# Kernel tuning notes

Hardware: AMD Instinct MI355X
Metric: run time of the kernel (lower is better)

The kernel has to match this reference:

```python
import jax, jax.numpy as jnp
import numpy as np

N = 50000   # nodes
E = 500000  # edges
DIN = 128
DOUT = 128
H = 8       # mulhead
DH = DOUT // H
L = 2       # layers per branch
NC = 7      # emotion classes
EPS = 1e-9  # BatchNorm eps from source


def _bn(x):
    # BatchNorm1d in train mode, gamma=1/beta=0 at init
    m = x.mean(axis=0)
    v = x.var(axis=0)
    return (x - m) * jax.lax.rsqrt(v + EPS)


def _gat_forward(f, row, col, vals, Ws, bs, Wn, bn, As, An):
    for i in range(L):
        hs = jax.nn.relu(jnp.einsum('nd,hdk->nhk', f, Ws[i]) + bs[i])  # [N,H,DH]
        hn = jax.nn.relu(jnp.einsum('nd,hdk->nhk', f, Wn[i]) + bn[i])  # [N,H,DH]
        ats = jax.nn.leaky_relu(jnp.einsum('nhk,hk->nh', hs, As[i]), negative_slope=0.2)  # [N,H]
        # NOTE: source computes attention_neigh from f_self (faithful)
        atn = jax.nn.leaky_relu(jnp.einsum('nhk,hk->nh', hs, An[i]), negative_slope=0.2)  # [N,H]
        e = (ats[row] + atn[col]) * vals[:, None]            # [E,H] per-edge attention
        msg = e[:, :, None] * hn[col]                        # [E,H,DH] gather + weight
        agg = jax.ops.segment_sum(msg, row, num_segments=N)  # [N,H,DH] scatter-add (sparse mm)
        f = _bn(agg.reshape(N, H * DH))                      # concat heads + norm
    return f


def _gcn_forward(f, row, col, vals, W, b):
    for i in range(L):
        h = f @ W[i] + b[i]                                  # [N,DOUT]
        agg = jax.ops.segment_sum(vals[:, None] * h[col], row, num_segments=N)
        f = _bn(jax.nn.relu(agg))
    return f


def setup_inputs() -> dict:
    key = jax.random.key(0)
    ks = jax.random.split(key, 24)
    inp = {}
    inp['f_in'] = jax.random.normal(ks[0], (N, DIN), jnp.float32)
    inp['edge_row'] = jax.random.randint(ks[1], (E,), 0, N, jnp.int32)
    inp['edge_col'] = jax.random.randint(ks[2], (E,), 0, N, jnp.int32)
    inp['vals_gat'] = jax.random.uniform(ks[3], (E,), jnp.float32)
    inp['vals_uttr'] = jax.random.uniform(ks[4], (E,), jnp.float32)
    inp['vals_past'] = jax.random.uniform(ks[5], (E,), jnp.float32)
    inp['vals_futr'] = jax.random.uniform(ks[6], (E,), jnp.float32)
    s = 0.05
    # GAT params (stacked over [layer, head]); layer0 in=DIN, later in=DOUT (equal here)
    inp['gat_Ws'] = jax.random.normal(ks[7], (L, H, DIN, DH), jnp.float32) * s
    inp['gat_bs'] = jnp.zeros((L, H, DH), jnp.float32)
    inp['gat_Wn'] = jax.random.normal(ks[8], (L, H, DIN, DH), jnp.float32) * s
    inp['gat_bn'] = jnp.zeros((L, H, DH), jnp.float32)
    inp['gat_as'] = jnp.ones((L, H, DH), jnp.float32)  # init ones per source
    inp['gat_an'] = jnp.ones((L, H, DH), jnp.float32)
    # three vanilla GCN branches
    inp['W_uttr'] = jax.random.normal(ks[9], (L, DIN, DOUT), jnp.float32) * s
    inp['b_uttr'] = jnp.zeros((L, DOUT), jnp.float32)
    inp['W_past'] = jax.random.normal(ks[10], (L, DIN, DOUT), jnp.float32) * s
    inp['b_past'] = jnp.zeros((L, DOUT), jnp.float32)
    inp['W_futr'] = jax.random.normal(ks[11], (L, DIN, DOUT), jnp.float32) * s
    inp['b_futr'] = jnp.zeros((L, DOUT), jnp.float32)
    # self perceptron + classifier
    inp['W_self'] = jax.random.normal(ks[12], (DIN, DOUT), jnp.float32) * s
    inp['b_self'] = jnp.zeros((DOUT,), jnp.float32)
    inp['W_cls'] = jax.random.normal(ks[13], (5 * DOUT, NC), jnp.float32) * s
    inp['b_cls'] = jnp.zeros((NC,), jnp.float32)
    return inp


def reference(f_in, edge_row, edge_col, vals_gat, vals_uttr, vals_past, vals_futr,
              gat_Ws, gat_bs, gat_Wn, gat_bn, gat_as, gat_an,
              W_uttr, b_uttr, W_past, b_past, W_futr, b_futr,
              W_self, b_self, W_cls, b_cls):
    o_gat = _gat_forward(f_in, edge_row, edge_col, vals_gat,
                         gat_Ws, gat_bs, gat_Wn, gat_bn, gat_as, gat_an)
    o_uttr = _gcn_forward(f_in, edge_row, edge_col, vals_uttr, W_uttr, b_uttr)
    o_past = _gcn_forward(f_in, edge_row, edge_col, vals_past, W_past, b_past)
    o_futr = _gcn_forward(f_in, edge_row, edge_col, vals_futr, W_futr, b_futr)
    o_self = _bn(jax.nn.relu(f_in @ W_self + b_self))
    f = jnp.concatenate([o_gat, o_uttr, o_past, o_futr, o_self], axis=1)  # [N,640]
    return f @ W_cls + b_cls  # classifier: act=False, plain linear
```

## Files before the change

kernel.cpp:

```cpp
#include <hip/hip_runtime.h>
#include <hip/hip_bf16.h>


#define NN 50000
#define NE 500000
#define DD 128
#define NH 8
#define DHD 16
#define NCLS 7
#define SCAN_B 196

typedef __attribute__((ext_vector_type(8))) short short8;
typedef __attribute__((ext_vector_type(4))) float f32x4;

__device__ __forceinline__ unsigned short f2bf(float x) {
    unsigned int u = __float_as_uint(x);
    unsigned int r = (u + 0x7fffu + ((u >> 16) & 1u)) >> 16;
    return (unsigned short)r;
}
__device__ __forceinline__ unsigned int pack2bf(float lo, float hi) {
    return (unsigned int)f2bf(lo) | ((unsigned int)f2bf(hi) << 16);
}
__device__ __forceinline__ float bflo(unsigned int u) { return __uint_as_float(u << 16); }
__device__ __forceinline__ float bfhi(unsigned int u) { return __uint_as_float(u & 0xffff0000u); }


__global__ void count_kernel(const int* __restrict__ row, int* __restrict__ cnt) {
    int e = blockIdx.x * 256 + threadIdx.x;
    if (e < NE) atomicAdd(&cnt[row[e]], 1);
}

__global__ __launch_bounds__(256) void scan1_kernel(const int* __restrict__ cnt,
                                                    int* __restrict__ pre,
                                                    int* __restrict__ bsum) {
    __shared__ int s[256];
    int t = threadIdx.x;
    int i = blockIdx.x * 256 + t;
    int v = (i < NN) ? cnt[i] : 0;
    s[t] = v;
    __syncthreads();
    for (int off = 1; off < 256; off <<= 1) {
        int u = (t >= off) ? s[t - off] : 0;
        __syncthreads();
        s[t] += u;
        __syncthreads();
    }
    if (i < NN) pre[i] = s[t] - v;
    if (t == 255) bsum[blockIdx.x] = s[255];
}

__global__ __launch_bounds__(256) void scan2_kernel(const int* __restrict__ bsum,
                                                    int* __restrict__ boff) {
    __shared__ int s[256];
    int t = threadIdx.x;
    int v = (t < SCAN_B) ? bsum[t] : 0;
    s[t] = v;
    __syncthreads();
    for (int off = 1; off < 256; off <<= 1) {
        int u = (t >= off) ? s[t - off] : 0;
        __syncthreads();
        s[t] += u;
        __syncthreads();
    }
    boff[t] = s[t] - v;
    if (t == 255) boff[256] = s[255];
}

__global__ __launch_bounds__(256) void scan3_kernel(const int* __restrict__ pre,
                                                    const int* __restrict__ boff,
                                                    int* __restrict__ row_ptr,
                                                    int* __restrict__ fill) {
    int t = threadIdx.x;
    int i = blockIdx.x * 256 + t;
    if (i < NN) {
        int v = pre[i] + boff[blockIdx.x];
        row_ptr[i] = v;
        fill[i] = v;
    }
    if (blockIdx.x == 0 && t == 0) row_ptr[NN] = boff[256];
}

__global__ void scatter_kernel(const int* __restrict__ row, const int* __restrict__ col,
                               const float* __restrict__ vg, const float* __restrict__ vu,
                               const float* __restrict__ vp, const float* __restrict__ vf,
                               int* __restrict__ fill, int4* __restrict__ ed) {
    int e = blockIdx.x * 256 + threadIdx.x;
    if (e >= NE) return;
    int r = row[e];
    int pos = atomicAdd(&fill[r], 1);
    ed[2 * pos] = make_int4(col[e], __float_as_int(vg[e]), __float_as_int(vu[e]),
                            __float_as_int(vp[e]));
    ed[2 * pos + 1] = make_int4(__float_as_int(vf[e]), 0, 0, 0);
}


__global__ __launch_bounds__(256) void tobf16_kernel(const float* __restrict__ x,
                                                     short* __restrict__ y) {
    int idx = blockIdx.x * 256 + threadIdx.x;
    if (idx >= NN * DD / 8) return;
    float4 a = ((const float4*)x)[idx * 2];
    float4 b = ((const float4*)x)[idx * 2 + 1];
    uint4 o;
    o.x = pack2bf(a.x, a.y);
    o.y = pack2bf(a.z, a.w);
    o.z = pack2bf(b.x, b.y);
    o.w = pack2bf(b.z, b.w);
    *(uint4*)(y + (size_t)idx * 8) = o;
}


struct WPrepArgs {
    const float* src[11];
};

__global__ __launch_bounds__(256) void wprep_kernel(WPrepArgs a, short* __restrict__ out) {
    int idx = blockIdx.x * 256 + threadIdx.x;
    if (idx >= 11 * DD * DD) return;
    int w = idx >> 14;
    int r = idx & 16383;
    int n = r >> 7, k = r & 127;
    const float* W = a.src[w];
    float v = (w < 4) ? W[(size_t)((n >> 4) * DD + k) * DHD + (n & 15)] : W[(size_t)k * DD + n];
    out[idx] = (short)f2bf(v);
}


struct WFixArgs {
    const float* W1[3];
    const float* b1[3];
    const float* stats[3];
};

__global__ __launch_bounds__(256) void wfix_kernel(WFixArgs a, short* __restrict__ wt_out,
                                                   float* __restrict__ bfix) {
    int idx = blockIdx.x * 256 + threadIdx.x;
    if (idx >= 3 * DD) return;
    int br = idx >> 7, n = idx & 127;
    const float* st = a.stats[br];
    const float* W = a.W1[br];
    const float inv_n = 1.0f / (float)NN;
    float accb = 0.f;
    short* wo = wt_out + (size_t)br * DD * DD + (size_t)n * DD;
#pragma unroll 4
    for (int k = 0; k < DD; ++k) {
        float m = st[k] * inv_n;
        float var = st[DD + k] * inv_n - m * m;
        float s = rsqrtf(var + 1e-9f);
        float w = W[(size_t)k * DD + n];
        wo[k] = (short)f2bf(s * w);
        accb += m * s * w;
    }
    bfix[idx] = a.b1[br][n] - accb;
}


__global__ __launch_bounds__(256) void mfma_mm_self(const short* __restrict__ A,
                                                    const short* __restrict__ Wt,
                                                    const float* __restrict__ bias,
                                                    float* __restrict__ stats_out,
                                                    float* __restrict__ C) {
    __shared__ short As[64 * DD];
    int t = threadIdx.x;
    int r0 = blockIdx.x * 64;
    {
        int srow = t >> 2;
        int sk0 = (t & 3) * 32;
        int grow = r0 + srow;
#pragma unroll
        for (int j = 0; j < 4; ++j) {
            int k0 = sk0 + j * 8;
            short8 frag = {0, 0, 0, 0, 0, 0, 0, 0};
            if (grow < NN) frag = *(const short8*)(A + (size_t)grow * DD + k0);
            int byte = srow * 256 + k0 * 2;
            byte ^= (srow & 7) << 4;
            *(short8*)((char*)As + byte) = frag;
        }
    }
    __syncthreads();
    int w = t >> 6, l = t & 63;
    int c0 = w * 32;
    int lr = l & 15, lg = l >> 4;
    f32x4 acc[4][2] = {};
#pragma unroll
    for (int s = 0; s < 4; ++s) {
        short8 af[4];
#pragma unroll
        for (int f = 0; f < 4; ++f) {
            int rr = f * 16 + lr;
            int byte = rr * 256 + (s * 32 + lg * 8) * 2;
            byte ^= (rr & 7) << 4;
            af[f] = *(const short8*)((const char*)As + byte);
        }
#pragma unroll
        for (int g = 0; g < 2; ++g) {
            int col = c0 + g * 16 + lr;
            short8 bf = *(const short8*)&Wt[(size_t)col * DD + s * 32 + lg * 8];
#pragma unroll
            for (int f = 0; f < 4; ++f)
                acc[f][g] = __builtin_amdgcn_mfma_f32_16x16x32_bf16(af[f], bf, acc[f][g], 0, 0, 0);
        }
    }
    float sA[2] = {0.f, 0.f}, qA[2] = {0.f, 0.f};
#pragma unroll
    for (int g = 0; g < 2; ++g) {
        int col = c0 + g * 16 + lr;
        float b = bias[col];
#pragma unroll
        for (int f = 0; f < 4; ++f)
#pragma unroll
            for (int i = 0; i < 4; ++i) {
                int row = r0 + f * 16 + lg * 4 + i;
                if (row < NN) {
                    float o = fmaxf(acc[f][g][i] + b, 0.f);
                    C[(size_t)row * DD + col] = o;
                    sA[g] += o;
                    qA[g] += o * o;
                }
            }
    }
#pragma unroll
    for (int g = 0; g < 2; ++g) {
        sA[g] += __shfl_xor(sA[g], 16);
        sA[g] += __shfl_xor(sA[g], 32);
        qA[g] += __shfl_xor(qA[g], 16);
        qA[g] += __shfl_xor(qA[g], 32);
    }
    if (lg == 0)
#pragma unroll
        for (int g = 0; g < 2; ++g) {
            int col = c0 + g * 16 + lr;
            atomicAdd(&stats_out[col], sA[g]);
            atomicAdd(&stats_out[DD + col], qA[g]);
        }
}


struct MMB {
    const short* A[3];
    const short* W[3];
    const float* bias[3];
    const float* rs[3];
    float* stats[3];
    short* C[3];
};

__global__ __launch_bounds__(256) void mfma_mm_gcn(MMB m) {
    int br = blockIdx.y;
    const short* A = m.A[br];
    const short* Wt = m.W[br];
    const float* bias = m.bias[br];
    const float* rs = m.rs[br];
    float* stats_out = m.stats[br];
    short* C = m.C[br];

    __shared__ short As[64 * DD];
    int t = threadIdx.x;
    int r0 = blockIdx.x * 64;
    {
        int srow = t >> 2;
        int sk0 = (t & 3) * 32;
        int grow = r0 + srow;
#pragma unroll
        for (int j = 0; j < 4; ++j) {
            int k0 = sk0 + j * 8;
            short8 frag = {0, 0, 0, 0, 0, 0, 0, 0};
            if (grow < NN) frag = *(const short8*)(A + (size_t)grow * DD + k0);
            int byte = srow * 256 + k0 * 2;
            byte ^= (srow & 7) << 4;
            *(short8*)((char*)As + byte) = frag;
        }
    }
    __syncthreads();
    int w = t >> 6, l = t & 63;
    int c0 = w * 32;
    int lr = l & 15, lg = l >> 4;
    f32x4 acc[4][2] = {};
#pragma unroll
    for (int s = 0; s < 4; ++s) {
        short8 af[4];
#pragma unroll
        for (int f = 0; f < 4; ++f) {
            int rr = f * 16 + lr;
            int byte = rr * 256 + (s * 32 + lg * 8) * 2;
            byte ^= (rr & 7) << 4;
            af[f] = *(const short8*)((const char*)As + byte);
        }
#pragma unroll
        for (int g = 0; g < 2; ++g) {
            int col = c0 + g * 16 + lr;
            short8 bf = *(const short8*)&Wt[(size_t)col * DD + s * 32 + lg * 8];
#pragma unroll
            for (int f = 0; f < 4; ++f)
                acc[f][g] = __builtin_amdgcn_mfma_f32_16x16x32_bf16(af[f], bf, acc[f][g], 0, 0, 0);
        }
    }
    float rsv[4][4];
#pragma unroll
    for (int f = 0; f < 4; ++f)
#pragma unroll
        for (int i = 0; i < 4; ++i) {
            int row = r0 + f * 16 + lg * 4 + i;
            rsv[f][i] = (row < NN) ? rs[row] : 0.f;
        }
    float sA[2] = {0.f, 0.f}, qA[2] = {0.f, 0.f};
#pragma unroll
    for (int g = 0; g < 2; ++g) {
        int col = c0 + g * 16 + lr;
        float b = bias[col];
#pragma unroll
        for (int f = 0; f < 4; ++f)
#pragma unroll
            for (int i = 0; i < 4; ++i) {
                int row = r0 + f * 16 + lg * 4 + i;
                if (row < NN) {
                    float o = fmaxf(acc[f][g][i] + rsv[f][i] * b, 0.f);
                    C[(size_t)row * DD + col] = (short)f2bf(o);
                    sA[g] += o;
                    qA[g] += o * o;
                }
            }
    }
#pragma unroll
    for (int g = 0; g < 2; ++g) {
        sA[g] += __shfl_xor(sA[g], 16);
        sA[g] += __shfl_xor(sA[g], 32);
        qA[g] += __shfl_xor(qA[g], 16);
        qA[g] += __shfl_xor(qA[g], 32);
    }
    if (lg == 0)
#pragma unroll
        for (int g = 0; g < 2; ++g) {
            int col = c0 + g * 16 + lr;
            atomicAdd(&stats_out[col], sA[g]);
            atomicAdd(&stats_out[DD + col], qA[g]);
        }
}


template <int PRE>
__global__ __launch_bounds__(256) void mfma_mm_pair(const void* __restrict__ Av,
                                                    const short* __restrict__ Wt1,
                                                    const short* __restrict__ Wt2,
                                                    const float* __restrict__ b1,
                                                    const float* __restrict__ b2,
                                                    const float* __restrict__ a_se,
                                                    const float* __restrict__ a_ne,
                                                    const float* __restrict__ stats_in,
                                                    short* __restrict__ out2,
                                                    float* __restrict__ ats_o,
                                                    float* __restrict__ atn_o) {
    __shared__ short As[64 * DD];
    __shared__ float mS[DD], sS[DD];
    int t = threadIdx.x;
    int r0 = blockIdx.x * 64;
    if (PRE == 1) {
        if (t < DD) {
            const float inv_n = 1.0f / (float)NN;
            float m = stats_in[t] * inv_n;
            float var = stats_in[DD + t] * inv_n - m * m;
            mS[t] = m;
            sS[t] = rsqrtf(var + 1e-9f);
        }
        __syncthreads();
    }
    {
        int srow = t >> 2;
        int sk0 = (t & 3) * 32;
        int grow = r0 + srow;
#pragma unroll
        for (int j = 0; j < 4; ++j) {
            int k0 = sk0 + j * 8;
            short8 frag = {0, 0, 0, 0, 0, 0, 0, 0};
            if (grow < NN) {
                if (PRE == 0) {
                    frag = *(const short8*)((const short*)Av + (size_t)grow * DD + k0);
                } else {
                    const float* Ar = (const float*)Av + (size_t)grow * DD;
                    float4 v0 = *(const float4*)(Ar + k0);
                    float4 v1 = *(const float4*)(Ar + k0 + 4);
                    float vv[8] = {v0.x, v0.y, v0.z, v0.w, v1.x, v1.y, v1.z, v1.w};
#pragma unroll
                    for (int e = 0; e < 8; ++e)
                        frag[e] = (short)f2bf((vv[e] - mS[k0 + e]) * sS[k0 + e]);
                }
            }
            int byte = srow * 256 + k0 * 2;
            byte ^= (srow & 7) << 4;
            *(short8*)((char*)As + byte) = frag;
        }
    }
    __syncthreads();
    int w = t >> 6, l = t & 63;
    int c0 = w * 32;
    int lr = l & 15, lg = l >> 4;
    f32x4 acc1[4][2] = {}, acc2[4][2] = {};
#pragma unroll
    for (int s = 0; s < 4; ++s) {
        short8 af[4];
#pragma unroll
        for (int f = 0; f < 4; ++f) {
            int rr = f * 16 + lr;
            int byte = rr * 256 + (s * 32 + lg * 8) * 2;
            byte ^= (rr & 7) << 4;
            af[f] = *(const short8*)((const char*)As + byte);
        }
#pragma unroll
        for (int g = 0; g < 2; ++g) {
            int col = c0 + g * 16 + lr;
            short8 bfa = *(const short8*)&Wt1[(size_t)col * DD + s * 32 + lg * 8];
            short8 bfb = *(const short8*)&Wt2[(size_t)col * DD + s * 32 + lg * 8];
#pragma unroll
            for (int f = 0; f < 4; ++f) {
                acc1[f][g] = __builtin_amdgcn_mfma_f32_16x16x32_bf16(af[f], bfa, acc1[f][g], 0, 0, 0);
                acc2[f][g] = __builtin_amdgcn_mfma_f32_16x16x32_bf16(af[f], bfb, acc2[f][g], 0, 0, 0);
            }
        }
    }
#pragma unroll
    for (int g = 0; g < 2; ++g) {
        int colc = c0 + g * 16 + lr;
        float bb1 = b1[colc], bb2 = b2[colc];
        float asv = a_se[colc], anv = a_ne[colc];
        int h = (c0 >> 4) + g;
#pragma unroll
        for (int f = 0; f < 4; ++f)
#pragma unroll
            for (int i = 0; i < 4; ++i) {
                int row = r0 + f * 16 + lg * 4 + i;
                float o1 = fmaxf(acc1[f][g][i] + bb1, 0.f);
                float o2 = fmaxf(acc2[f][g][i] + bb2, 0.f);
                if (row < NN) out2[(size_t)row * DD + colc] = (short)f2bf(o2);
                float ds = o1 * asv, dn = o1 * anv;
                ds += __shfl_xor(ds, 1);
                dn += __shfl_xor(dn, 1);
                ds += __shfl_xor(ds, 2);
                dn += __shfl_xor(dn, 2);
                ds += __shfl_xor(ds, 4);
                dn += __shfl_xor(dn, 4);
                ds += __shfl_xor(ds, 8);
                dn += __shfl_xor(dn, 8);
                if (lr == 0 && row < NN) {
                    ats_o[row * NH + h] = ds > 0.f ? ds : 0.2f * ds;
                    atn_o[row * NH + h] = dn > 0.f ? dn : 0.2f * dn;
                }
            }
    }
}


__global__ __launch_bounds__(256) void spmm_fusedA(
    const short* __restrict__ hnb, const short* __restrict__ fbf, const float* __restrict__ ats,
    const float* __restrict__ atn, const int4* __restrict__ ed, const int* __restrict__ row_ptr,
    float* __restrict__ aggG, short* __restrict__ zu, short* __restrict__ zp,
    short* __restrict__ zf, float* __restrict__ rs_all) {
    int r = __builtin_amdgcn_readfirstlane((blockIdx.x * 256 + threadIdx.x) >> 6);
    int lane = threadIdx.x & 63;
    if (r >= NN) return;
    int hh = lane >> 3;
    float a_s = ats[r * NH + hh];
    int start = row_ptr[r], end = row_ptr[r + 1];
    float2 ag = {0.f, 0.f}, au = {0.f, 0.f}, ap = {0.f, 0.f}, af2 = {0.f, 0.f};
    float su = 0.f, sp = 0.f, sf = 0.f;
    int j = start;
    for (; j + 2 <= end; j += 2) {
        int4 a0 = ed[2 * j], b0 = ed[2 * j + 1];
        int4 a1 = ed[2 * j + 2], b1 = ed[2 * j + 3];
        int cA = a0.x, cB = a1.x;
        float at0 = atn[cA * NH + hh], at1 = atn[cB * NH + hh];
        unsigned int g0 = *(const unsigned int*)(hnb + (size_t)cA * DD + lane * 2);
        unsigned int f0 = *(const unsigned int*)(fbf + (size_t)cA * DD + lane * 2);
        unsigned int g1 = *(const unsigned int*)(hnb + (size_t)cB * DD + lane * 2);
        unsigned int f1 = *(const unsigned int*)(fbf + (size_t)cB * DD + lane * 2);
        {
            float vg = __int_as_float(a0.y), vu = __int_as_float(a0.z);
            float vp = __int_as_float(a0.w), vf = __int_as_float(b0.x);
            float e = (a_s + at0) * vg;
            float glo = bflo(g0), ghi = bfhi(g0), flo = bflo(f0), fhi = bfhi(f0);
            ag.x += e * glo;  ag.y += e * ghi;
            au.x += vu * flo; au.y += vu * fhi;
            ap.x += vp * flo; ap.y += vp * fhi;
            af2.x += vf * flo; af2.y += vf * fhi;
            su += vu; sp += vp; sf += vf;
        }
        {
            float vg = __int_as_float(a1.y), vu = __int_as_float(a1.z);
            float vp = __int_as_float(a1.w), vf = __int_as_float(b1.x);
            float e = (a_s + at1) * vg;
            float glo = bflo(g1), ghi = bfhi(g1), flo = bflo(f1), fhi = bfhi(f1);
            ag.x += e * glo;  ag.y += e * ghi;
            au.x += vu * flo; au.y += vu * fhi;
            ap.x += vp * flo; ap.y += vp * fhi;
            af2.x += vf * flo; af2.y += vf * fhi;
            su += vu; sp += vp; sf += vf;
        }
    }
    if (j < end) {
        int4 a0 = ed[2 * j], b0 = ed[2 * j + 1];
        int cA = a0.x;
        float at0 = atn[cA * NH + hh];
        unsigned int g0 = *(const unsigned int*)(hnb + (size_t)cA * DD + lane * 2);
        unsigned int f0 = *(const unsigned int*)(fbf + (size_t)cA * DD + lane * 2);
        float vg = __int_as_float(a0.y), vu = __int_as_float(a0.z);
        float vp = __int_as_float(a0.w), vf = __int_as_float(b0.x);
        float e = (a_s + at0) * vg;
        float glo = bflo(g0), ghi = bfhi(g0), flo = bflo(f0), fhi = bfhi(f0);
        ag.x += e * glo;  ag.y += e * ghi;
        au.x += vu * flo; au.y += vu * fhi;
        ap.x += vp * flo; ap.y += vp * fhi;
        af2.x += vf * flo; af2.y += vf * fhi;
        su += vu; sp += vp; sf += vf;
    }
    size_t o = (size_t)r * DD + lane * 2;
    *(float2*)&aggG[o] = ag;
    *(unsigned int*)(zu + o) = pack2bf(au.x, au.y);
    *(unsigned int*)(zp + o) = pack2bf(ap.x, ap.y);
    *(unsigned int*)(zf + o) = pack2bf(af2.x, af2.y);
    if (lane == 0) {
        rs_all[r] = su;
        rs_all[NN + r] = sp;
        rs_all[2 * NN + r] = sf;
    }
}


__global__ __launch_bounds__(256) void spmm_fusedB(
    const short* __restrict__ hnb, const short* __restrict__ y0u, const short* __restrict__ y0p,
    const short* __restrict__ y0f, const float* __restrict__ ats, const float* __restrict__ atn,
    const int4* __restrict__ ed, const int* __restrict__ row_ptr, float* __restrict__ aggG,
    short* __restrict__ z1u, short* __restrict__ z1p, short* __restrict__ z1f) {
    int r = __builtin_amdgcn_readfirstlane((blockIdx.x * 256 + threadIdx.x) >> 6);
    int lane = threadIdx.x & 63;
    if (r >= NN) return;
    int hh = lane >> 3;
    float a_s = ats[r * NH + hh];
    int start = row_ptr[r], end = row_ptr[r + 1];
    float2 ag = {0.f, 0.f}, au = {0.f, 0.f}, ap = {0.f, 0.f}, af2 = {0.f, 0.f};
    int j = start;
    for (; j + 2 <= end; j += 2) {
        int4 a0 = ed[2 * j], b0 = ed[2 * j + 1];
        int4 a1 = ed[2 * j + 2], b1 = ed[2 * j + 3];
        int cA = a0.x, cB = a1.x;
        float at0 = atn[cA * NH + hh], at1 = atn[cB * NH + hh];
        size_t oA = (size_t)cA * DD + lane * 2, oB = (size_t)cB * DD + lane * 2;
        unsigned int g0 = *(const unsigned int*)(hnb + oA);
        unsigned int u0 = *(const unsigned int*)(y0u + oA);
        unsigned int p0 = *(const unsigned int*)(y0p + oA);
        unsigned int q0 = *(const unsigned int*)(y0f + oA);
        unsigned int g1 = *(const unsigned int*)(hnb + oB);
        unsigned int u1 = *(const unsigned int*)(y0u + oB);
        unsigned int p1 = *(const unsigned int*)(y0p + oB);
        unsigned int q1 = *(const unsigned int*)(y0f + oB);
        float e0 = (a_s + at0) * __int_as_float(a0.y);
        float e1 = (a_s + at1) * __int_as_float(a1.y);
        float vu0 = __int_as_float(a0.z), vp0 = __int_as_float(a0.w), vf0 = __int_as_float(b0.x);
        float vu1 = __int_as_float(a1.z), vp1 = __int_as_float(a1.w), vf1 = __int_as_float(b1.x);
        ag.x += e0 * bflo(g0) + e1 * bflo(g1);
        ag.y += e0 * bfhi(g0) + e1 * bfhi(g1);
        au.x += vu0 * bflo(u0) + vu1 * bflo(u1);
        au.y += vu0 * bfhi(u0) + vu1 * bfhi(u1);
        ap.x += vp0 * bflo(p0) + vp1 * bflo(p1);
        ap.y += vp0 * bfhi(p0) + vp1 * bfhi(p1);
        af2.x += vf0 * bflo(q0) + vf1 * bflo(q1);
        af2.y += vf0 * bfhi(q0) + vf1 * bfhi(q1);
    }
    if (j < end) {
        int4 a0 = ed[2 * j], b0 = ed[2 * j + 1];
        int cA = a0.x;
        float at0 = atn[cA * NH + hh];
        size_t oA = (size_t)cA * DD + lane * 2;
        unsigned int g0 = *(const unsigned int*)(hnb + oA);
        unsigned int u0 = *(const unsigned int*)(y0u + oA);
        unsigned int p0 = *(const unsigned int*)(y0p + oA);
        unsigned int q0 = *(const unsigned int*)(y0f + oA);
        float e0 = (a_s + at0) * __int_as_float(a0.y);
        float vu0 = __int_as_float(a0.z), vp0 = __int_as_float(a0.w), vf0 = __int_as_float(b0.x);
        ag.x += e0 * bflo(g0);
        ag.y += e0 * bfhi(g0);
        au.x += vu0 * bflo(u0);
        au.y += vu0 * bfhi(u0);
        ap.x += vp0 * bflo(p0);
        ap.y += vp0 * bfhi(p0);
        af2.x += vf0 * bflo(q0);
        af2.y += vf0 * bfhi(q0);
    }
    size_t o = (size_t)r * DD + lane * 2;
    *(float2*)&aggG[o] = ag;
    *(unsigned int*)(z1u + o) = pack2bf(au.x, au.y);
    *(unsigned int*)(z1p + o) = pack2bf(ap.x, ap.y);
    *(unsigned int*)(z1f + o) = pack2bf(af2.x, af2.y);
}


__global__ __launch_bounds__(256) void bn_stats_kernel(const float* __restrict__ x,
                                                       float* __restrict__ stats) {
    int c = threadIdx.x & 127;
    int sub = threadIdx.x >> 7;
    int rows_per_block = (NN + gridDim.x - 1) / gridDim.x;
    int rbeg = blockIdx.x * rows_per_block;
    int rend = min(rbeg + rows_per_block, NN);
    float s = 0.f, q = 0.f;
    for (int r = rbeg + sub; r < rend; r += 2) {
        float v = x[(size_t)r * DD + c];
        s += v;
        q += v * v;
    }
    atomicAdd(&stats[c], s);
    atomicAdd(&stats[DD + c], q);
}


template <int PRE, bool FIRST, bool BF16IN>
__global__ __launch_bounds__(256) void cls_acc_kernel(const void* __restrict__ ov,
                                                      const float* __restrict__ Wc,
                                                      const float* __restrict__ stats,
                                                      const float* __restrict__ b_cls,
                                                      float* __restrict__ out) {
    __shared__ float Wl[DD * NCLS];
    __shared__ float mS[DD], sS[DD];
    int t = threadIdx.x;
    for (int i = t; i < DD * NCLS; i += 256) Wl[i] = Wc[i];
    if (PRE && t < DD) {
        const float inv_n = 1.0f / (float)NN;
        float m = stats[t] * inv_n;
        float var = stats[DD + t] * inv_n - m * m;
        mS[t] = m;
        sS[t] = rsqrtf(var + 1e-9f);
    }
    __syncthreads();
    int n = blockIdx.x * 256 + t;
    if (n >= NN) return;
    float acc[NCLS] = {};
    if (BF16IN) {
        const uint4* orow = (const uint4*)((const short*)ov + (size_t)n * DD);
        for (int k8 = 0; k8 < DD / 8; ++k8) {
            uint4 v = orow[k8];
            float vv[8] = {bflo(v.x), bfhi(v.x), bflo(v.y), bfhi(v.y),
                           bflo(v.z), bfhi(v.z), bflo(v.w), bfhi(v.w)};
#pragma unroll
            for (int kk = 0; kk < 8; ++kk) {
                int k = k8 * 8 + kk;
                float a = vv[kk];
                if (PRE == 2) a = fmaxf(a, 0.f);
                if (PRE) a = (a - mS[k]) * sS[k];
#pragma unroll
                for (int c = 0; c < NCLS; ++c) acc[c] += a * Wl[k * NCLS + c];
            }
        }
    } else {
        const float4* orow = (const float4*)((const float*)ov + (size_t)n * DD);
        for (int k4 = 0; k4 < DD / 4; ++k4) {
            float4 v = orow[k4];
#pragma unroll
            for (int kk = 0; kk < 4; ++kk) {
                int k = k4 * 4 + kk;
                float a = ((const float*)&v)[kk];
                if (PRE == 2) a = fmaxf(a, 0.f);
                if (PRE) a = (a - mS[k]) * sS[k];
#pragma unroll
                for (int c = 0; c < NCLS; ++c) acc[c] += a * Wl[k * NCLS + c];
            }
        }
    }
#pragma unroll
    for (int c = 0; c < NCLS; ++c) {
        if (FIRST)
            out[n * NCLS + c] = acc[c] + b_cls[c];
        else
            out[n * NCLS + c] += acc[c];
    }
}


extern "C" void kernel_launch(void* const* d_in, const int* in_sizes, int n_in, void* d_out,
                              int out_size, void* d_ws, size_t ws_size, hipStream_t stream) {
    const float* f_in = (const float*)d_in[0];
    const int* edge_row = (const int*)d_in[1];
    const int* edge_col = (const int*)d_in[2];
    const float* vals_gat = (const float*)d_in[3];
    const float* vals_uttr = (const float*)d_in[4];
    const float* vals_past = (const float*)d_in[5];
    const float* vals_futr = (const float*)d_in[6];
    const float* gat_Ws = (const float*)d_in[7];
    const float* gat_bs = (const float*)d_in[8];
    const float* gat_Wn = (const float*)d_in[9];
    const float* gat_bn = (const float*)d_in[10];
    const float* gat_as = (const float*)d_in[11];
    const float* gat_an = (const float*)d_in[12];
    const float* W_uttr = (const float*)d_in[13];
    const float* b_uttr = (const float*)d_in[14];
    const float* W_past = (const float*)d_in[15];
    const float* b_past = (const float*)d_in[16];
    const float* W_futr = (const float*)d_in[17];
    const float* b_futr = (const float*)d_in[18];
    const float* W_self = (const float*)d_in[19];
    const float* b_self = (const float*)d_in[20];
    const float* W_cls = (const float*)d_in[21];
    const float* b_cls = (const float*)d_in[22];
    float* out = (float*)d_out;

    char* ws = (char*)d_ws;
    size_t off = 0;
    auto alloc = [&](size_t bytes) -> void* {
        void* p = ws + off;
        off = (off + bytes + 255) & ~(size_t)255;
        return p;
    };
    float* stats_all = (float*)alloc(9 * 2 * DD * 4);
    int* cnt = (int*)alloc((size_t)NN * 4);
    float* tmp1 = (float*)alloc((size_t)NN * DD * 4);
    float* bufA = (float*)alloc((size_t)NN * DD * 4);
    short* fbf = (short*)alloc((size_t)NN * DD * 2);
    short* hnb = (short*)alloc((size_t)NN * DD * 2);
    short* z0u = (short*)alloc((size_t)NN * DD * 2);
    short* z0p = (short*)alloc((size_t)NN * DD * 2);
    short* z0f = (short*)alloc((size_t)NN * DD * 2);
    float* rs_all = (float*)alloc((size_t)3 * NN * 4);
    float* ats_b = (float*)alloc((size_t)NN * NH * 4);
    float* atn_b = (float*)alloc((size_t)NN * NH * 4);
    short* Wt_all = (short*)alloc((size_t)14 * DD * DD * 2);
    float* bfix = (float*)alloc((size_t)3 * DD * 4);
    int* row_ptr = (int*)alloc((size_t)(NN + 1) * 4);
    int* fill = (int*)alloc((size_t)NN * 4);
    int* pre_b = (int*)alloc((size_t)NN * 4);
    int* bsum = (int*)alloc((size_t)SCAN_B * 4);
    int* boff = (int*)alloc((size_t)257 * 4);
    int4* ed = (int4*)alloc((size_t)NE * 32);

    auto stats = [&](int s) { return stats_all + (size_t)s * 2 * DD; };
    auto Wt = [&](int w) { return Wt_all + (size_t)w * DD * DD; };

    const int gE = (NE + 255) / 256;
    const int gMM = (NN + 63) / 64;
    const int gSP = (NN + 3) / 4;
    const int gCA = (NN + 255) / 256;
    const int gBF = (NN * DD / 8 + 255) / 256;

    hipMemsetAsync(stats_all, 0, 9 * 2 * DD * 4 + (size_t)NN * 4, stream);

    count_kernel<<<gE, 256, 0, stream>>>(edge_row, cnt);
    scan1_kernel<<<SCAN_B, 256, 0, stream>>>(cnt, pre_b, bsum);
    scan2_kernel<<<1, 256, 0, stream>>>(bsum, boff);
    scan3_kernel<<<SCAN_B, 256, 0, stream>>>(pre_b, boff, row_ptr, fill);
    scatter_kernel<<<gE, 256, 0, stream>>>(edge_row, edge_col, vals_gat, vals_uttr, vals_past,
                                           vals_futr, fill, ed);

    tobf16_kernel<<<gBF, 256, 0, stream>>>(f_in, fbf);

    WPrepArgs wa;
    wa.src[0] = gat_Ws;
    wa.src[1] = gat_Wn;
    wa.src[2] = gat_Ws + (size_t)DD * DD;
    wa.src[3] = gat_Wn + (size_t)DD * DD;
    wa.src[4] = W_uttr;
    wa.src[5] = W_uttr + (size_t)DD * DD;
    wa.src[6] = W_past;
    wa.src[7] = W_past + (size_t)DD * DD;
    wa.src[8] = W_futr;
    wa.src[9] = W_futr + (size_t)DD * DD;
    wa.src[10] = W_self;
    wprep_kernel<<<(11 * DD * DD + 255) / 256, 256, 0, stream>>>(wa, Wt_all);

    mfma_mm_self<<<gMM, 256, 0, stream>>>(fbf, Wt(10), b_self, stats(8), tmp1);
    cls_acc_kernel<1, true, false><<<gCA, 256, 0, stream>>>(tmp1, W_cls + (size_t)4 * DD * NCLS,
                                                            stats(8), b_cls, out);

    mfma_mm_pair<0><<<gMM, 256, 0, stream>>>(fbf, Wt(0), Wt(1), gat_bs, gat_bn, gat_as, gat_an,
                                             nullptr, hnb, ats_b, atn_b);
    spmm_fusedA<<<gSP, 256, 0, stream>>>(hnb, fbf, ats_b, atn_b, ed, row_ptr, bufA, z0u, z0p,
                                         z0f, rs_all);
    bn_stats_kernel<<<256, 256, 0, stream>>>(bufA, stats(0));
    mfma_mm_pair<1><<<gMM, 256, 0, stream>>>(bufA, Wt(2), Wt(3), gat_bs + DD, gat_bn + DD,
                                             gat_as + DD, gat_an + DD, stats(0), hnb, ats_b,
                                             atn_b);

    const float* bb[3] = {b_uttr, b_past, b_futr};
    const float* Worig[3] = {W_uttr, W_past, W_futr};
    MMB m0;
    short* z0a[3] = {z0u, z0p, z0f};
    for (int br = 0; br < 3; ++br) {
        m0.A[br] = z0a[br];
        m0.W[br] = Wt(4 + br * 2);
        m0.bias[br] = bb[br];
        m0.rs[br] = rs_all + (size_t)br * NN;
        m0.stats[br] = stats(2 + br);
        m0.C[br] = z0a[br];
    }
    mfma_mm_gcn<<<dim3(gMM, 3), 256, 0, stream>>>(m0);

    WFixArgs wf;
    for (int br = 0; br < 3; ++br) {
        wf.W1[br] = Worig[br] + (size_t)DD * DD;
        wf.b1[br] = bb[br] + DD;
        wf.stats[br] = stats(2 + br);
    }
    wfix_kernel<<<2, 256, 0, stream>>>(wf, Wt(11), bfix);

    short* z1u = fbf;
    short* z1p = (short*)tmp1;
    short* z1f = (short*)tmp1 + (size_t)NN * DD;
    spmm_fusedB<<<gSP, 256, 0, stream>>>(hnb, z0u, z0p, z0f, ats_b, atn_b, ed, row_ptr, bufA,
                                         z1u, z1p, z1f);
    bn_stats_kernel<<<256, 256, 0, stream>>>(bufA, stats(1));
    cls_acc_kernel<1, false, false><<<gCA, 256, 0, stream>>>(bufA, W_cls, stats(1), b_cls, out);

    MMB m1;
    short* z1a[3] = {z1u, z1p, z1f};
    for (int br = 0; br < 3; ++br) {
        m1.A[br] = z1a[br];
        m1.W[br] = Wt(11 + br);
        m1.bias[br] = bfix + (size_t)br * DD;
        m1.rs[br] = rs_all + (size_t)br * NN;
        m1.stats[br] = stats(5 + br);
        m1.C[br] = z0a[br];
    }
    mfma_mm_gcn<<<dim3(gMM, 3), 256, 0, stream>>>(m1);

    for (int br = 0; br < 3; ++br)
        cls_acc_kernel<1, false, true><<<gCA, 256, 0, stream>>>(
            z0a[br], W_cls + (size_t)(DD + DD * br) * NCLS, stats(5 + br), b_cls, out);
}
```

Measured before the change: 572.8 us.

## Interleave gather sources per node and fuse BN stats into SpMM

Stores the features gathered per neighbor (hn plus f, or hn plus the three GCN branch outputs) in one interleaved per-node buffer, so each edge needs a single wide load instead of 2-4 narrow ones. It also folds the BatchNorm column statistics into the SpMM kernels through shared-memory atomics, removing the separate bn_stats passes. The three per-branch classifier launches are merged into one 2D-grid launch. In exchange there are extra strided bf16 writes into the interleaved buffers from tobf16 and the GEMM epilogues, plus shared and global atomics in the SpMM.

New measurement: 1.043 ms. +82.1%, slower.

```diff
diff --git a/kernel.cpp b/kernel.cpp
--- a/kernel.cpp
+++ b/kernel.cpp
@@ -95,9 +95,12 @@
 
 
 __global__ __launch_bounds__(256) void tobf16_kernel(const float* __restrict__ x,
-                                                     short* __restrict__ y) {
+                                                     short* __restrict__ y,
+                                                     char* __restrict__ G2) {
     int idx = blockIdx.x * 256 + threadIdx.x;
     if (idx >= NN * DD / 8) return;
+    int node = idx >> 4;
+    int k0 = (idx & 15) * 8;
     float4 a = ((const float4*)x)[idx * 2];
     float4 b = ((const float4*)x)[idx * 2 + 1];
     uint4 o;
@@ -106,6 +109,11 @@
     o.z = pack2bf(b.x, b.y);
     o.w = pack2bf(b.z, b.w);
     *(uint4*)(y + (size_t)idx * 8) = o;
+    char* g = G2 + (size_t)node * 512 + (k0 >> 1) * 8;
+    *(unsigned int*)(g) = o.x;
+    *(unsigned int*)(g + 8) = o.y;
+    *(unsigned int*)(g + 16) = o.z;
+    *(unsigned int*)(g + 24) = o.w;
 }
 
 
@@ -241,7 +249,8 @@
     const float* bias[3];
     const float* rs[3];
     float* stats[3];
-    short* C[3];
+    char* C[3];
+    int rowb, pairb;
 };
 
 __global__ __launch_bounds__(256) void mfma_mm_gcn(MMB m) {
@@ -251,7 +260,8 @@
     const float* bias = m.bias[br];
     const float* rs = m.rs[br];
     float* stats_out = m.stats[br];
-    short* C = m.C[br];
+    char* C = m.C[br];
+    int rowb = m.rowb, pairb = m.pairb;
 
     __shared__ short As[64 * DD];
     int t = threadIdx.x;
@@ -307,6 +317,7 @@
     for (int g = 0; g < 2; ++g) {
         int col = c0 + g * 16 + lr;
         float b = bias[col];
+        size_t cb = (size_t)(col >> 1) * pairb + (col & 1) * 2;
 #pragma unroll
         for (int f = 0; f < 4; ++f)
 #pragma unroll
@@ -314,7 +325,7 @@
                 int row = r0 + f * 16 + lg * 4 + i;
                 if (row < NN) {
                     float o = fmaxf(acc[f][g][i] + rsv[f][i] * b, 0.f);
-                    C[(size_t)row * DD + col] = (short)f2bf(o);
+                    *(short*)(C + (size_t)row * rowb + cb) = (short)f2bf(o);
                     sA[g] += o;
                     qA[g] += o * o;
                 }
@@ -346,8 +357,8 @@
                                                     const float* __restrict__ a_se,
                                                     const float* __restrict__ a_ne,
                                                     const float* __restrict__ stats_in,
-                                                    short* __restrict__ out2,
-                                                    float* __restrict__ ats_o,
+                                                    char* __restrict__ out2base, int rowb,
+                                                    int pairb, float* __restrict__ ats_o,
                                                     float* __restrict__ atn_o) {
     __shared__ short As[64 * DD];
     __shared__ float mS[DD], sS[DD];
@@ -422,6 +433,7 @@
         float bb1 = b1[colc], bb2 = b2[colc];
         float asv = a_se[colc], anv = a_ne[colc];
         int h = (c0 >> 4) + g;
+        size_t cb = (size_t)(colc >> 1) * pairb + (colc & 1) * 2;
 #pragma unroll
         for (int f = 0; f < 4; ++f)
 #pragma unroll
@@ -429,7 +441,7 @@
                 int row = r0 + f * 16 + lg * 4 + i;
                 float o1 = fmaxf(acc1[f][g][i] + bb1, 0.f);
                 float o2 = fmaxf(acc2[f][g][i] + bb2, 0.f);
-                if (row < NN) out2[(size_t)row * DD + colc] = (short)f2bf(o2);
+                if (row < NN) *(short*)(out2base + (size_t)row * rowb + cb) = (short)f2bf(o2);
                 float ds = o1 * asv, dn = o1 * anv;
                 ds += __shfl_xor(ds, 1);
                 dn += __shfl_xor(dn, 1);
@@ -449,13 +461,16 @@
 
 
 __global__ __launch_bounds__(256) void spmm_fusedA(
-    const short* __restrict__ hnb, const short* __restrict__ fbf, const float* __restrict__ ats,
-    const float* __restrict__ atn, const int4* __restrict__ ed, const int* __restrict__ row_ptr,
-    float* __restrict__ aggG, short* __restrict__ zu, short* __restrict__ zp,
-    short* __restrict__ zf, float* __restrict__ rs_all) {
-    int r = __builtin_amdgcn_readfirstlane((blockIdx.x * 256 + threadIdx.x) >> 6);
-    int lane = threadIdx.x & 63;
-    if (r >= NN) return;
+    const char* __restrict__ G2, const float* __restrict__ ats, const float* __restrict__ atn,
+    const int4* __restrict__ ed, const int* __restrict__ row_ptr, float* __restrict__ aggG,
+    short* __restrict__ zu, short* __restrict__ zp, short* __restrict__ zf,
+    float* __restrict__ rs_all, float* __restrict__ stats0) {
+    __shared__ float sred[2 * DD];
+    int t = threadIdx.x;
+    sred[t] = 0.f;
+    __syncthreads();
+    int r = __builtin_amdgcn_readfirstlane((blockIdx.x * 256 + t) >> 6);
+    int lane = t & 63;
     int hh = lane >> 3;
     float a_s = ats[r * NH + hh];
     int start = row_ptr[r], end = row_ptr[r + 1];
@@ -467,15 +482,13 @@
         int4 a1 = ed[2 * j + 2], b1 = ed[2 * j + 3];
         int cA = a0.x, cB = a1.x;
         float at0 = atn[cA * NH + hh], at1 = atn[cB * NH + hh];
-        unsigned int g0 = *(const unsigned int*)(hnb + (size_t)cA * DD + lane * 2);
-        unsigned int f0 = *(const unsigned int*)(fbf + (size_t)cA * DD + lane * 2);
-        unsigned int g1 = *(const unsigned int*)(hnb + (size_t)cB * DD + lane * 2);
-        unsigned int f1 = *(const unsigned int*)(fbf + (size_t)cB * DD + lane * 2);
+        uint2 d0 = *(const uint2*)(G2 + (size_t)cA * 512 + lane * 8);
+        uint2 d1 = *(const uint2*)(G2 + (size_t)cB * 512 + lane * 8);
         {
             float vg = __int_as_float(a0.y), vu = __int_as_float(a0.z);
             float vp = __int_as_float(a0.w), vf = __int_as_float(b0.x);
             float e = (a_s + at0) * vg;
-            float glo = bflo(g0), ghi = bfhi(g0), flo = bflo(f0), fhi = bfhi(f0);
+            float flo = bflo(d0.x), fhi = bfhi(d0.x), glo = bflo(d0.y), ghi = bfhi(d0.y);
             ag.x += e * glo;  ag.y += e * ghi;
             au.x += vu * flo; au.y += vu * fhi;
             ap.x += vp * flo; ap.y += vp * fhi;
@@ -486,7 +499,7 @@
             float vg = __int_as_float(a1.y), vu = __int_as_float(a1.z);
             float vp = __int_as_float(a1.w), vf = __int_as_float(b1.x);
             float e = (a_s + at1) * vg;
-            float glo = bflo(g1), ghi = bfhi(g1), flo = bflo(f1), fhi = bfhi(f1);
+            float flo = bflo(d1.x), fhi = bfhi(d1.x), glo = bflo(d1.y), ghi = bfhi(d1.y);
             ag.x += e * glo;  ag.y += e * ghi;
             au.x += vu * flo; au.y += vu * fhi;
             ap.x += vp * flo; ap.y += vp * fhi;
@@ -498,12 +511,11 @@
         int4 a0 = ed[2 * j], b0 = ed[2 * j + 1];
         int cA = a0.x;
         float at0 = atn[cA * NH + hh];
-        unsigned int g0 = *(const unsigned int*)(hnb + (size_t)cA * DD + lane * 2);
-        unsigned int f0 = *(const unsigned int*)(fbf + (size_t)cA * DD + lane * 2);
+        uint2 d0 = *(const uint2*)(G2 + (size_t)cA * 512 + lane * 8);
         float vg = __int_as_float(a0.y), vu = __int_as_float(a0.z);
         float vp = __int_as_float(a0.w), vf = __int_as_float(b0.x);
         float e = (a_s + at0) * vg;
-        float glo = bflo(g0), ghi = bfhi(g0), flo = bflo(f0), fhi = bfhi(f0);
+        float flo = bflo(d0.x), fhi = bfhi(d0.x), glo = bflo(d0.y), ghi = bfhi(d0.y);
         ag.x += e * glo;  ag.y += e * ghi;
         au.x += vu * flo; au.y += vu * fhi;
         ap.x += vp * flo; ap.y += vp * fhi;
@@ -520,17 +532,26 @@
         rs_all[NN + r] = sp;
         rs_all[2 * NN + r] = sf;
     }
+    atomicAdd(&sred[2 * lane], ag.x);
+    atomicAdd(&sred[2 * lane + 1], ag.y);
+    atomicAdd(&sred[DD + 2 * lane], ag.x * ag.x);
+    atomicAdd(&sred[DD + 2 * lane + 1], ag.y * ag.y);
+    __syncthreads();
+    atomicAdd(&stats0[t], sred[t]);
 }
 
 
 __global__ __launch_bounds__(256) void spmm_fusedB(
-    const short* __restrict__ hnb, const short* __restrict__ y0u, const short* __restrict__ y0p,
-    const short* __restrict__ y0f, const float* __restrict__ ats, const float* __restrict__ atn,
+    const char* __restrict__ G4, const float* __restrict__ ats, const float* __restrict__ atn,
     const int4* __restrict__ ed, const int* __restrict__ row_ptr, float* __restrict__ aggG,
-    short* __restrict__ z1u, short* __restrict__ z1p, short* __restrict__ z1f) {
-    int r = __builtin_amdgcn_readfirstlane((blockIdx.x * 256 + threadIdx.x) >> 6);
-    int lane = threadIdx.x & 63;
-    if (r >= NN) return;
+    short* __restrict__ z1u, short* __restrict__ z1p, short* __restrict__ z1f,
+    float* __restrict__ stats1) {
+    __shared__ float sred[2 * DD];
+    int t = threadIdx.x;
+    sred[t] = 0.f;
+    __syncthreads();
+    int r = __builtin_amdgcn_readfirstlane((blockIdx.x * 256 + t) >> 6);
+    int lane = t & 63;
     int hh = lane >> 3;
     float a_s = ats[r * NH + hh];
     int start = row_ptr[r], end = row_ptr[r + 1];
@@ -541,76 +562,53 @@
         int4 a1 = ed[2 * j + 2], b1 = ed[2 * j + 3];
         int cA = a0.x, cB = a1.x;
         float at0 = atn[cA * NH + hh], at1 = atn[cB * NH + hh];
-        size_t oA = (size_t)cA * DD + lane * 2, oB = (size_t)cB * DD + lane * 2;
-        unsigned int g0 = *(const unsigned int*)(hnb + oA);
-        unsigned int u0 = *(const unsigned int*)(y0u + oA);
-        unsigned int p0 = *(const unsigned int*)(y0p + oA);
-        unsigned int q0 = *(const unsigned int*)(y0f + oA);
-        unsigned int g1 = *(const unsigned int*)(hnb + oB);
-        unsigned int u1 = *(const unsigned int*)(y0u + oB);
-        unsigned int p1 = *(const unsigned int*)(y0p + oB);
-        unsigned int q1 = *(const unsigned int*)(y0f + oB);
+        uint4 d0 = *(const uint4*)(G4 + (size_t)cA * 1024 + lane * 16);
+        uint4 d1 = *(const uint4*)(G4 + (size_t)cB * 1024 + lane * 16);
         float e0 = (a_s + at0) * __int_as_float(a0.y);
         float e1 = (a_s + at1) * __int_as_float(a1.y);
         float vu0 = __int_as_float(a0.z), vp0 = __int_as_float(a0.w), vf0 = __int_as_float(b0.x);
         float vu1 = __int_as_float(a1.z), vp1 = __int_as_float(a1.w), vf1 = __int_as_float(b1.x);
-        ag.x += e0 * bflo(g0) + e1 * bflo(g1);
-        ag.y += e0 * bfhi(g0) + e1 * bfhi(g1);
-        au.x += vu0 * bflo(u0) + vu1 * bflo(u1);
-        au.y += vu0 * bfhi(u0) + vu1 * bfhi(u1);
-        ap.x += vp0 * bflo(p0) + vp1 * bflo(p1);
-        ap.y += vp0 * bfhi(p0) + vp1 * bfhi(p1);
-        af2.x += vf0 * bflo(q0) + vf1 * bflo(q1);
-        af2.y += vf0 * bfhi(q0) + vf1 * bfhi(q1);
+        ag.x += e0 * bflo(d0.x) + e1 * bflo(d1.x);
+        ag.y += e0 * bfhi(d0.x) + e1 * bfhi(d1.x);
+        au.x += vu0 * bflo(d0.y) + vu1 * bflo(d1.y);
+        au.y += vu0 * bfhi(d0.y) + vu1 * bfhi(d1.y);
+        ap.x += vp0 * bflo(d0.z) + vp1 * bflo(d1.z);
+        ap.y += vp0 * bfhi(d0.z) + vp1 * bfhi(d1.z);
+        af2.x += vf0 * bflo(d0.w) + vf1 * bflo(d1.w);
+        af2.y += vf0 * bfhi(d0.w) + vf1 * bfhi(d1.w);
     }
     if (j < end) {
         int4 a0 = ed[2 * j], b0 = ed[2 * j + 1];
         int cA = a0.x;
         float at0 = atn[cA * NH + hh];
-        size_t oA = (size_t)cA * DD + lane * 2;
-        unsigned int g0 = *(const unsigned int*)(hnb + oA);
-        unsigned int u0 = *(const unsigned int*)(y0u + oA);
-        unsigned int p0 = *(const unsigned int*)(y0p + oA);
-        unsigned int q0 = *(const unsigned int*)(y0f + oA);
+        uint4 d0 = *(const uint4*)(G4 + (size_t)cA * 1024 + lane * 16);
         float e0 = (a_s + at0) * __int_as_float(a0.y);
         float vu0 = __int_as_float(a0.z), vp0 = __int_as_float(a0.w), vf0 = __int_as_float(b0.x);
-        ag.x += e0 * bflo(g0);
-        ag.y += e0 * bfhi(g0);
-        au.x += vu0 * bflo(u0);
-        au.y += vu0 * bfhi(u0);
-        ap.x += vp0 * bflo(p0);
-        ap.y += vp0 * bfhi(p0);
-        af2.x += vf0 * bflo(q0);
-        af2.y += vf0 * bfhi(q0);
+        ag.x += e0 * bflo(d0.x);
+        ag.y += e0 * bfhi(d0.x);
+        au.x += vu0 * bflo(d0.y);
+        au.y += vu0 * bfhi(d0.y);
+        ap.x += vp0 * bflo(d0.z);
+        ap.y += vp0 * bfhi(d0.z);
+        af2.x += vf0 * bflo(d0.w);
+        af2.y += vf0 * bfhi(d0.w);
     }
     size_t o = (size_t)r * DD + lane * 2;
     *(float2*)&aggG[o] = ag;
     *(unsigned int*)(z1u + o) = pack2bf(au.x, au.y);
     *(unsigned int*)(z1p + o) = pack2bf(ap.x, ap.y);
     *(unsigned int*)(z1f + o) = pack2bf(af2.x, af2.y);
-}
-
-
-__global__ __launch_bounds__(256) void bn_stats_kernel(const float* __restrict__ x,
-                                                       float* __restrict__ stats) {
-    int c = threadIdx.x & 127;
-    int sub = threadIdx.x >> 7;
-    int rows_per_block = (NN + gridDim.x - 1) / gridDim.x;
-    int rbeg = blockIdx.x * rows_per_block;
-    int rend = min(rbeg + rows_per_block, NN);
-    float s = 0.f, q = 0.f;
-    for (int r = rbeg + sub; r < rend; r += 2) {
-        float v = x[(size_t)r * DD + c];
-        s += v;
-        q += v * v;
-    }
-    atomicAdd(&stats[c], s);
-    atomicAdd(&stats[DD + c], q);
-}
-
-
-template <int PRE, bool FIRST, bool BF16IN>
-__global__ __launch_bounds__(256) void cls_acc_kernel(const void* __restrict__ ov,
+    atomicAdd(&sred[2 * lane], ag.x);
+    atomicAdd(&sred[2 * lane + 1], ag.y);
+    atomicAdd(&sred[DD + 2 * lane], ag.x * ag.x);
+    atomicAdd(&sred[DD + 2 * lane + 1], ag.y * ag.y);
+    __syncthreads();
+    atomicAdd(&stats1[t], sred[t]);
+}
+
+
+template <bool FIRST>
+__global__ __launch_bounds__(256) void cls_acc_kernel(const float* __restrict__ o,
                                                       const float* __restrict__ Wc,
                                                       const float* __restrict__ stats,
                                                       const float* __restrict__ b_cls,
@@ -619,7 +617,7 @@
     __shared__ float mS[DD], sS[DD];
     int t = threadIdx.x;
     for (int i = t; i < DD * NCLS; i += 256) Wl[i] = Wc[i];
-    if (PRE && t < DD) {
+    if (t < DD) {
         const float inv_n = 1.0f / (float)NN;
         float m = stats[t] * inv_n;
         float var = stats[DD + t] * inv_n - m * m;
@@ -630,35 +628,15 @@
     int n = blockIdx.x * 256 + t;
     if (n >= NN) return;
     float acc[NCLS] = {};
-    if (BF16IN) {
-        const uint4* orow = (const uint4*)((const short*)ov + (size_t)n * DD);
-        for (int k8 = 0; k8 < DD / 8; ++k8) {
-            uint4 v = orow[k8];
-            float vv[8] = {bflo(v.x), bfhi(v.x), bflo(v.y), bfhi(v.y),
-                           bflo(v.z), bfhi(v.z), bflo(v.w), bfhi(v.w)};
-#pragma unroll
-            for (int kk = 0; kk < 8; ++kk) {
-                int k = k8 * 8 + kk;
-                float a = vv[kk];
-                if (PRE == 2) a = fmaxf(a, 0.f);
-                if (PRE) a = (a - mS[k]) * sS[k];
-#pragma unroll
-                for (int c = 0; c < NCLS; ++c) acc[c] += a * Wl[k * NCLS + c];
-            }
-        }
-    } else {
-        const float4* orow = (const float4*)((const float*)ov + (size_t)n * DD);
-        for (int k4 = 0; k4 < DD / 4; ++k4) {
-            float4 v = orow[k4];
-#pragma unroll
-            for (int kk = 0; kk < 4; ++kk) {
-                int k = k4 * 4 + kk;
-                float a = ((const float*)&v)[kk];
-                if (PRE == 2) a = fmaxf(a, 0.f);
-                if (PRE) a = (a - mS[k]) * sS[k];
-#pragma unroll
-                for (int c = 0; c < NCLS; ++c) acc[c] += a * Wl[k * NCLS + c];
-            }
+    const float4* orow = (const float4*)(o + (size_t)n * DD);
+    for (int k4 = 0; k4 < DD / 4; ++k4) {
+        float4 v = orow[k4];
+#pragma unroll
+        for (int kk = 0; kk < 4; ++kk) {
+            int k = k4 * 4 + kk;
+            float a = (((const float*)&v)[kk] - mS[k]) * sS[k];
+#pragma unroll
+            for (int c = 0; c < NCLS; ++c) acc[c] += a * Wl[k * NCLS + c];
         }
     }
 #pragma unroll
@@ -668,6 +646,50 @@
         else
             out[n * NCLS + c] += acc[c];
     }
+}
+
+
+struct CLS3 {
+    const short* o[3];
+    const float* stats[3];
+};
+
+__global__ __launch_bounds__(256) void cls3_kernel(CLS3 a, const float* __restrict__ W_cls,
+                                                   float* __restrict__ out) {
+    int br = blockIdx.y;
+    const short* o = a.o[br];
+    const float* st = a.stats[br];
+    const float* Wc = W_cls + (size_t)(DD + DD * br) * NCLS;
+    __shared__ float Wl[DD * NCLS];
+    __shared__ float mS[DD], sS[DD];
+    int t = threadIdx.x;
+    for (int i = t; i < DD * NCLS; i += 256) Wl[i] = Wc[i];
+    if (t < DD) {
+        const float inv_n = 1.0f / (float)NN;
+        float m = st[t] * inv_n;
+        float var = st[DD + t] * inv_n - m * m;
+        mS[t] = m;
+        sS[t] = rsqrtf(var + 1e-9f);
+    }
+    __syncthreads();
+    int n = blockIdx.x * 256 + t;
+    if (n >= NN) return;
+    float acc[NCLS] = {};
+    const uint4* orow = (const uint4*)(o + (size_t)n * DD);
+    for (int k8 = 0; k8 < DD / 8; ++k8) {
+        uint4 v = orow[k8];
+        float vv[8] = {bflo(v.x), bfhi(v.x), bflo(v.y), bfhi(v.y),
+                       bflo(v.z), bfhi(v.z), bflo(v.w), bfhi(v.w)};
+#pragma unroll
+        for (int kk = 0; kk < 8; ++kk) {
+            int k = k8 * 8 + kk;
+            float a2 = (vv[kk] - mS[k]) * sS[k];
+#pragma unroll
+            for (int c = 0; c < NCLS; ++c) acc[c] += a2 * Wl[k * NCLS + c];
+        }
+    }
+#pragma unroll
+    for (int c = 0; c < NCLS; ++c) atomicAdd(&out[n * NCLS + c], acc[c]);
 }
 
 
@@ -710,7 +732,8 @@
     float* tmp1 = (float*)alloc((size_t)NN * DD * 4);
     float* bufA = (float*)alloc((size_t)NN * DD * 4);
     short* fbf = (short*)alloc((size_t)NN * DD * 2);
-    short* hnb = (short*)alloc((size_t)NN * DD * 2);
+    char* G2 = (char*)alloc((size_t)NN * 512);
+    char* G4 = (char*)alloc((size_t)NN * 1024);
     short* z0u = (short*)alloc((size_t)NN * DD * 2);
     short* z0p = (short*)alloc((size_t)NN * DD * 2);
     short* z0f = (short*)alloc((size_t)NN * DD * 2);
@@ -731,7 +754,7 @@
 
     const int gE = (NE + 255) / 256;
     const int gMM = (NN + 63) / 64;
-    const int gSP = (NN + 3) / 4;
+    const int gSP = NN / 4;
     const int gCA = (NN + 255) / 256;
     const int gBF = (NN * DD / 8 + 255) / 256;
 
@@ -744,7 +767,7 @@
     scatter_kernel<<<gE, 256, 0, stream>>>(edge_row, edge_col, vals_gat, vals_uttr, vals_past,
                                            vals_futr, fill, ed);
 
-    tobf16_kernel<<<gBF, 256, 0, stream>>>(f_in, fbf);
+    tobf16_kernel<<<gBF, 256, 0, stream>>>(f_in, fbf, G2);
 
     WPrepArgs wa;
     wa.src[0] = gat_Ws;
@@ -761,30 +784,32 @@
     wprep_kernel<<<(11 * DD * DD + 255) / 256, 256, 0, stream>>>(wa, Wt_all);
 
     mfma_mm_self<<<gMM, 256, 0, stream>>>(fbf, Wt(10), b_self, stats(8), tmp1);
-    cls_acc_kernel<1, true, false><<<gCA, 256, 0, stream>>>(tmp1, W_cls + (size_t)4 * DD * NCLS,
-                                                            stats(8), b_cls, out);
+    cls_acc_kernel<true><<<gCA, 256, 0, stream>>>(tmp1, W_cls + (size_t)4 * DD * NCLS, stats(8),
+                                                  b_cls, out);
 
     mfma_mm_pair<0><<<gMM, 256, 0, stream>>>(fbf, Wt(0), Wt(1), gat_bs, gat_bn, gat_as, gat_an,
-                                             nullptr, hnb, ats_b, atn_b);
-    spmm_fusedA<<<gSP, 256, 0, stream>>>(hnb, fbf, ats_b, atn_b, ed, row_ptr, bufA, z0u, z0p,
-                                         z0f, rs_all);
-    bn_stats_kernel<<<256, 256, 0, stream>>>(bufA, stats(0));
+                                             nullptr, G2 + 4, 512, 8, ats_b, atn_b);
+    spmm_fusedA<<<gSP, 256, 0, stream>>>(G2, ats_b, atn_b, ed, row_ptr, bufA, z0u, z0p, z0f,
+                                         rs_all, stats(0));
+
     mfma_mm_pair<1><<<gMM, 256, 0, stream>>>(bufA, Wt(2), Wt(3), gat_bs + DD, gat_bn + DD,
-                                             gat_as + DD, gat_an + DD, stats(0), hnb, ats_b,
-                                             atn_b);
+                                             gat_as + DD, gat_an + DD, stats(0), G4, 1024, 16,
+                                             ats_b, atn_b);
 
     const float* bb[3] = {b_uttr, b_past, b_futr};
     const float* Worig[3] = {W_uttr, W_past, W_futr};
+    short* z0a[3] = {z0u, z0p, z0f};
     MMB m0;
-    short* z0a[3] = {z0u, z0p, z0f};
     for (int br = 0; br < 3; ++br) {
         m0.A[br] = z0a[br];
         m0.W[br] = Wt(4 + br * 2);
         m0.bias[br] = bb[br];
         m0.rs[br] = rs_all + (size_t)br * NN;
         m0.stats[br] = stats(2 + br);
-        m0.C[br] = z0a[br];
-    }
+        m0.C[br] = G4 + 4 + br * 4;
+    }
+    m0.rowb = 1024;
+    m0.pairb = 16;
     mfma_mm_gcn<<<dim3(gMM, 3), 256, 0, stream>>>(m0);
 
     WFixArgs wf;
@@ -798,10 +823,9 @@
     short* z1u = fbf;
     short* z1p = (short*)tmp1;
     short* z1f = (short*)tmp1 + (size_t)NN * DD;
-    spmm_fusedB<<<gSP, 256, 0, stream>>>(hnb, z0u, z0p, z0f, ats_b, atn_b, ed, row_ptr, bufA,
-                                         z1u, z1p, z1f);
-    bn_stats_kernel<<<256, 256, 0, stream>>>(bufA, stats(1));
-    cls_acc_kernel<1, false, false><<<gCA, 256, 0, stream>>>(bufA, W_cls, stats(1), b_cls, out);
+    spmm_fusedB<<<gSP, 256, 0, stream>>>(G4, ats_b, atn_b, ed, row_ptr, bufA, z1u, z1p, z1f,
+                                         stats(1));
+    cls_acc_kernel<false><<<gCA, 256, 0, stream>>>(bufA, W_cls, stats(1), b_cls, out);
 
     MMB m1;
     short* z1a[3] = {z1u, z1p, z1f};
@@ -811,11 +835,16 @@
         m1.bias[br] = bfix + (size_t)br * DD;
         m1.rs[br] = rs_all + (size_t)br * NN;
         m1.stats[br] = stats(5 + br);
-        m1.C[br] = z0a[br];
-    }
+        m1.C[br] = (char*)z0a[br];
+    }
+    m1.rowb = 256;
+    m1.pairb = 4;
     mfma_mm_gcn<<<dim3(gMM, 3), 256, 0, stream>>>(m1);
 
-    for (int br = 0; br < 3; ++br)
-        cls_acc_kernel<1, false, true><<<gCA, 256, 0, stream>>>(
-            z0a[br], W_cls + (size_t)(DD + DD * br) * NCLS, stats(5 + br), b_cls, out);
-}
+    CLS3 c3;
+    for (int br = 0; br < 3; ++br) {
+        c3.o[br] = z0a[br];
+        c3.stats[br] = stats(5 + br);
+    }
+    cls3_kernel<<<dim3(gCA, 3), 256, 0, stream>>>(c3, W_cls, out);
+}
```
